# Optimization experiments

Hardware: AMD Instinct MI355X
Metric: run time of the kernel (lower is better)

## Reference

```python
import jax, jax.numpy as jnp
import numpy as np
from jax import lax

VOCAB = 32000
D = 256      # d_model
N = 16       # n_neurons
NL = 6       # n_layers
DS = 16      # d_state
DC = 4       # d_conv
DI = 512     # d_inner = expand * d_model
DTR = 16     # dt_rank = ceil(D/16)
NH = 4       # attention heads
HD = D // NH
B, L = 1, 128


def setup_inputs() -> dict:
    key = jax.random.key(0)
    ks = list(jax.random.split(key, 32))
    it = iter(ks)

    def rn(shape, scale):
        return jax.random.normal(next(it), shape, jnp.float32) * scale

    p = {}
    p["x"] = jax.random.randint(next(it), (B, L), 0, VOCAB, dtype=jnp.int32)
    p["embedding"] = rn((VOCAB, D), 0.02)
    p["norm1_w"] = jnp.ones((NL, D)); p["norm1_b"] = jnp.zeros((NL, D))
    p["norm2_w"] = jnp.ones((NL, D)); p["norm2_b"] = jnp.zeros((NL, D))
    # Mamba params (stacked over layers)
    p["in_proj_w"] = rn((NL, 2 * DI, D), D ** -0.5)
    p["conv_w"] = rn((NL, DI, DC), DC ** -0.5)
    p["conv_b"] = jnp.zeros((NL, DI))
    p["x_proj_w"] = rn((NL, DTR + 2 * DS, DI), DI ** -0.5)
    p["dt_proj_w"] = rn((NL, DI, DTR), DTR ** -0.5)
    dt0 = jax.random.uniform(next(it), (NL, DI), jnp.float32, 1e-3, 1e-1)
    p["dt_proj_b"] = jnp.log(jnp.expm1(dt0))  # inverse softplus init
    p["A_log"] = jnp.log(jnp.tile(jnp.arange(1.0, DS + 1.0, dtype=jnp.float32), (NL, DI, 1)))
    p["skip_D"] = jnp.ones((NL, DI))
    p["out_proj_w"] = rn((NL, D, DI), DI ** -0.5)
    # cross-neuron MHA params
    p["attn_in_w"] = rn((NL, 3 * D, D), D ** -0.5)
    p["attn_in_b"] = jnp.zeros((NL, 3 * D))
    p["attn_out_w"] = rn((NL, D, D), D ** -0.5)
    p["attn_out_b"] = jnp.zeros((NL, D))
    p["norm_f_w"] = jnp.ones((D,)); p["norm_f_b"] = jnp.zeros((D,))
    p["head_b"] = jnp.zeros((VOCAB,))
    return p


def _ln(x, w, b):
    m = x.mean(-1, keepdims=True)
    v = ((x - m) ** 2).mean(-1, keepdims=True)
    return (x - m) * lax.rsqrt(v + 1e-5) * w + b


def _mamba(x, ipw, cw, cb, xpw, dpw, dpb, alog, dskip, opw):
    # x: (BN, L, D)
    BN, Ls, _ = x.shape
    xz = x @ ipw.T                       # (BN, L, 2*DI)
    u, z = xz[..., :DI], xz[..., DI:]
    # depthwise causal conv1d, kernel DC, left-pad DC-1
    uc = lax.conv_general_dilated(
        u.swapaxes(1, 2), cw[:, None, :], (1,), [(DC - 1, 0)],
        dimension_numbers=("NCH", "OIH", "NCH"), feature_group_count=DI)
    u = jax.nn.silu(uc + cb[None, :, None]).swapaxes(1, 2)  # (BN, L, DI)
    xdbl = u @ xpw.T                     # (BN, L, DTR+2*DS)
    dt = jax.nn.softplus(xdbl[..., :DTR] @ dpw.T + dpb)     # (BN, L, DI)
    Bm = xdbl[..., DTR:DTR + DS]
    Cm = xdbl[..., DTR + DS:]
    A = -jnp.exp(alog)                   # (DI, DS)

    def step(h, ins):
        dt_t, b_t, c_t, u_t = ins        # (BN,DI) (BN,DS) (BN,DS) (BN,DI)
        h = jnp.exp(dt_t[..., None] * A) * h + (dt_t * u_t)[..., None] * b_t[:, None, :]
        return h, jnp.einsum("bds,bs->bd", h, c_t)

    h0 = jnp.zeros((BN, DI, DS), x.dtype)
    _, ys = lax.scan(step, h0, (dt.swapaxes(0, 1), Bm.swapaxes(0, 1),
                                Cm.swapaxes(0, 1), u.swapaxes(0, 1)))
    y = ys.swapaxes(0, 1) + u * dskip
    return (y * jax.nn.silu(z)) @ opw.T


def _mha(x, iw, ib, ow, ob):
    # x: (B*L, N, D); self-attention across neurons
    Bq, S, _ = x.shape
    qkv = x @ iw.T + ib
    q, k, v = jnp.split(qkv, 3, axis=-1)
    q = q.reshape(Bq, S, NH, HD); k = k.reshape(Bq, S, NH, HD); v = v.reshape(Bq, S, NH, HD)
    att = jax.nn.softmax(jnp.einsum("bqhd,bkhd->bhqk", q, k) / np.float32(np.sqrt(HD)), axis=-1)
    o = jnp.einsum("bhqk,bkhd->bqhd", att, v).reshape(Bq, S, D)
    return o @ ow.T + ob


def reference(x, embedding, norm1_w, norm1_b, norm2_w, norm2_b, in_proj_w, conv_w,
              conv_b, x_proj_w, dt_proj_w, dt_proj_b, A_log, skip_D, out_proj_w,
              attn_in_w, attn_in_b, attn_out_w, attn_out_b, norm_f_w, norm_f_b, head_b):
    Bb, Ll = x.shape
    h = embedding[x]                                             # (B, L, D)
    h = jnp.broadcast_to(h[:, None], (Bb, N, Ll, D)).reshape(Bb * N, Ll, D)
    for i in range(NL):
        h = h + _mamba(_ln(h, norm1_w[i], norm1_b[i]), in_proj_w[i], conv_w[i],
                       conv_b[i], x_proj_w[i], dt_proj_w[i], dt_proj_b[i],
                       A_log[i], skip_D[i], out_proj_w[i])
        xc = _ln(h, norm2_w[i], norm2_b[i]).reshape(Bb, N, Ll, D)
        xc = xc.transpose(0, 2, 1, 3).reshape(Bb * Ll, N, D)
        co = _mha(xc, attn_in_w[i], attn_in_b[i], attn_out_w[i], attn_out_b[i])
        h = h + co.reshape(Bb, Ll, N, D).transpose(0, 2, 1, 3).reshape(Bb * N, Ll, D)
    h = h.reshape(Bb, N, Ll, D).mean(axis=1)                     # avg over neurons
    return _ln(h, norm_f_w, norm_f_b) @ embedding.T + head_b     # tied head
```

## Files before the change

kernel.cpp:

```cpp
#include <hip/hip_runtime.h>

constexpr int SEQ    = 128;
constexpr int NVOCAB = 32000;

constexpr size_t O_HA = 0;
constexpr size_t O_HB = O_HA + (size_t)SEQ*256;
constexpr size_t O_U  = O_HB + (size_t)SEQ*256;
constexpr size_t O_DT = O_U  + (size_t)SEQ*512;
constexpr size_t O_ZS = O_DT + (size_t)SEQ*512;
constexpr size_t O_BC = O_ZS + (size_t)SEQ*512;
constexpr size_t O_YG = O_BC + (size_t)SEQ*32;
constexpr size_t O_AH = O_YG + (size_t)SEQ*512;

__device__ __forceinline__ float wsum(float p) {
    #pragma unroll
    for (int m = 1; m < 64; m <<= 1) p += __shfl_xor(p, m);
    return p;
}
__device__ __forceinline__ float dot4(float4 a, float4 b) {
    return a.x*b.x + a.y*b.y + a.z*b.z + a.w*b.w;
}

template<int MR, int KK, int S>
__device__ __forceinline__ void gemm3(
    const float* __restrict__ Wg, const float* __restrict__ A, int AS,
    float* __restrict__ dest, int DS,
    const float* __restrict__ addsrc, int ASS, const float* __restrict__ bias)
{
    constexpr int NST = KK / (4 * S);
    const int tid = threadIdx.x;
    const int tq  = tid & (S - 1);
    const int c0  = (tid / S) * 2;
    const float* Wp0 = Wg + (size_t)c0*KK + tq*4;
    const float* Wp1 = Wp0 + KK;

    float acc0[MR], acc1[MR];
    #pragma unroll
    for (int r = 0; r < MR; ++r) { acc0[r] = 0.f; acc1[r] = 0.f; }

    float4 wa0 = *(const float4*)(Wp0);
    float4 wa1 = *(const float4*)(Wp1);
    float4 wb0 = *(const float4*)(Wp0 + 4*S);
    float4 wb1 = *(const float4*)(Wp1 + 4*S);

    #pragma unroll 1
    for (int st = 0; st < NST; st += 2) {
        float4 na0, na1, nb0, nb1;
        const bool pa = (st + 2 < NST);
        const bool pb = (st + 3 < NST);
        if (pa) { na0 = *(const float4*)(Wp0 + (st+2)*4*S);
                  na1 = *(const float4*)(Wp1 + (st+2)*4*S); }
        if (pb) { nb0 = *(const float4*)(Wp0 + (st+3)*4*S);
                  nb1 = *(const float4*)(Wp1 + (st+3)*4*S); }
        const int k0 = st*4*S + tq*4;
        #pragma unroll
        for (int r = 0; r < MR; ++r) {
            float4 a = *(const float4*)&A[r*AS + k0];
            acc0[r] += dot4(a, wa0);
            acc1[r] += dot4(a, wa1);
        }
        const int k1 = k0 + 4*S;
        #pragma unroll
        for (int r = 0; r < MR; ++r) {
            float4 a = *(const float4*)&A[r*AS + k1];
            acc0[r] += dot4(a, wb0);
            acc1[r] += dot4(a, wb1);
        }
        if (pa) { wa0 = na0; wa1 = na1; }
        if (pb) { wb0 = nb0; wb1 = nb1; }
    }
    #pragma unroll
    for (int m = 1; m < S; m <<= 1) {
        #pragma unroll
        for (int r = 0; r < MR; ++r) {
            acc0[r] += __shfl_xor(acc0[r], m);
            acc1[r] += __shfl_xor(acc1[r], m);
        }
    }
    if (tq == 0) {
        #pragma unroll
        for (int r = 0; r < MR; ++r) {
            float ox = acc0[r], oy = acc1[r];
            if (bias) { ox += bias[c0]; oy += bias[c0+1]; }
            if (addsrc) {
                float2 s = *(const float2*)&addsrc[r*ASS + c0];
                ox += s.x; oy += s.y;
            }
            float2 o; o.x = ox; o.y = oy;
            *(float2*)&dest[r*DS + c0] = o;
        }
    }
}

__device__ __forceinline__ void ln_row(const float* __restrict__ src, float* __restrict__ dst,
                                       const float* __restrict__ w, const float* __restrict__ b)
{
    int lane = threadIdx.x & 63;
    float4 x = *(const float4*)&src[lane*4];
    float sm = wsum(x.x + x.y + x.z + x.w);
    float mean = sm * (1.0f/256.0f);
    float d0 = x.x-mean, d1 = x.y-mean, d2 = x.z-mean, d3 = x.w-mean;
    float var = wsum(d0*d0 + d1*d1 + d2*d2 + d3*d3) * (1.0f/256.0f);
    float rstd = rsqrtf(var + 1e-5f);
    float4 ww = *(const float4*)&w[lane*4];
    float4 bb = *(const float4*)&b[lane*4];
    float4 o;
    o.x = d0*rstd*ww.x + bb.x;
    o.y = d1*rstd*ww.y + bb.y;
    o.z = d2*rstd*ww.z + bb.z;
    o.w = d3*rstd*ww.w + bb.w;
    *(float4*)&dst[lane*4] = o;
}

__global__ __launch_bounds__(1024, 4) void rowk_kernel(
    const int* __restrict__ x, const float* __restrict__ emb,
    const float* __restrict__ n1w_l, const float* __restrict__ n1b_l,
    const float* __restrict__ n2w_l, const float* __restrict__ n2b_l,
    const float* __restrict__ ipw_l, const float* __restrict__ cw_l, const float* __restrict__ cb_l,
    const float* __restrict__ xpw_l, const float* __restrict__ dpw_l, const float* __restrict__ dpb_l,
    const float* __restrict__ opw_l, const float* __restrict__ aivw_l, const float* __restrict__ aivb_l,
    const float* __restrict__ aow_l, const float* __restrict__ aob_l,
    const float* __restrict__ nfw, const float* __restrict__ nfb,
    const float* __restrict__ hin, float* __restrict__ hout,
    const float* __restrict__ ygv, float* __restrict__ uv, float* __restrict__ dtv,
    float* __restrict__ zsv, float* __restrict__ bcv, float* __restrict__ AH,
    int li)
{
    __shared__ float SM[6336];
    float* hP  = SM;
    float* h1  = SM + 1056;
    float* sLN = SM + 2112;
    float* sAX = SM + 3168;
    float* zR  = SM + 5248;
    float* suR = SM + 5760;
    float* sxR = SM + 6272;

    const int r = blockIdx.x;
    const int tid = threadIdx.x;
    const int lane = tid & 63, wv = tid >> 6;
    int rr[4];
    #pragma unroll
    for (int j = 0; j < 4; ++j) { int v = r - 3 + j; rr[j] = v < 0 ? 0 : v; }

    {
        int hr = tid >> 8, hc = tid & 255;
        if (li <= 1) hP[hr*264 + hc] = emb[(size_t)x[rr[hr]]*256 + hc];
        else         hP[hr*264 + hc] = hin[rr[hr]*256 + hc];
    }
    if (li >= 1) {
        int yr = tid >> 9, yc = tid & 511;
        sAX[yr*520 + yc]     = ygv[rr[yr]*512 + yc];
        sAX[(2+yr)*520 + yc] = ygv[rr[2+yr]*512 + yc];
    }
    __syncthreads();

    float* hC = hP;
    if (li >= 1) {
        gemm3<4,512,8>(opw_l, sAX, 520, h1, 264, hP, 264, nullptr);
        __syncthreads();
        if (wv < 4) ln_row(h1 + wv*264, sLN + wv*264, n2w_l, n2b_l);
        __syncthreads();
        gemm3<4,256,8>(aivw_l, sLN, 264, sAX, 520, nullptr, 0, aivb_l);
        __syncthreads();
        gemm3<4,256,8>(aow_l, sAX, 520, h1, 264, h1, 264, aob_l);
        __syncthreads();
        hC = h1;
        if (tid < 256) hout[r*256 + tid] = h1[3*264 + tid];
        if (li == 6) {
            if (tid < 256) {
                float v = h1[3*264 + tid];
                float s = wsum(v);
                float q = wsum(v*v);
                if (lane == 0) { sxR[wv] = s; sxR[8 + wv] = q; }
            }
            __syncthreads();
            if (tid < 256) {
                float v = h1[3*264 + tid];
                float mean = (sxR[0]+sxR[1]+sxR[2]+sxR[3]) * (1.0f/256.0f);
                float var  = (sxR[8]+sxR[9]+sxR[10]+sxR[11]) * (1.0f/256.0f) - mean*mean;
                float rstd = rsqrtf(var + 1e-5f);
                AH[r*256 + tid] = (v - mean)*rstd*nfw[tid] + nfb[tid];
            }
            return;
        }
    }

    if (wv < 4) ln_row(hC + wv*264, sLN + wv*264, n1w_l, n1b_l);
    __syncthreads();
    gemm3<4,256,4>(ipw_l,                   sLN,         264, sAX, 520, nullptr, 0, nullptr);
    gemm3<1,256,4>(ipw_l + (size_t)512*256, sLN + 3*264, 264, zR,  512, nullptr, 0, nullptr);
    __syncthreads();

    if (tid < 512) {
        int d = tid;
        float4 c4 = *(const float4*)&cw_l[d*4];
        float acc = cb_l[d];
        if (r >= 3) acc += sAX[d]        * c4.x;
        if (r >= 2) acc += sAX[520 + d]  * c4.y;
        if (r >= 1) acc += sAX[1040 + d] * c4.z;
        acc += sAX[1560 + d] * c4.w;
        float sg = acc / (1.0f + __expf(-acc));
        suR[d] = sg;
        uv[r*512 + d] = sg;
        float z = zR[d];
        zsv[r*512 + d] = z / (1.0f + __expf(-z));
    }
    __syncthreads();

    {
        float4 a0 = *(const float4*)&suR[lane*4];
        float4 a1 = *(const float4*)&suR[256 + lane*4];
        float p[3];
        #pragma unroll
        for (int j = 0; j < 3; ++j) {
            int c = wv*3 + j;
            float4 q0 = *(const float4*)&xpw_l[(size_t)c*512 + lane*4];
            float4 q1 = *(const float4*)&xpw_l[(size_t)c*512 + 256 + lane*4];
            p[j] = dot4(a0, q0) + dot4(a1, q1);
        }
        #pragma unroll
        for (int m = 1; m < 64; m <<= 1) {
            #pragma unroll
            for (int j = 0; j < 3; ++j) p[j] += __shfl_xor(p[j], m);
        }
        if (lane == 0) {
            #pragma unroll
            for (int j = 0; j < 3; ++j) sxR[wv*3 + j] = p[j];
        }
    }
    __syncthreads();
    if (tid >= 16 && tid < 48) bcv[r*32 + tid - 16] = sxR[tid];

    if (tid < 512) {
        int d = tid;
        float4 sx0 = *(const float4*)&sxR[0];
        float4 sx1 = *(const float4*)&sxR[4];
        float4 sx2 = *(const float4*)&sxR[8];
        float4 sx3 = *(const float4*)&sxR[12];
        const float4* dp = (const float4*)&dpw_l[(size_t)d*16];
        float acc = dpb_l[d] + dot4(dp[0], sx0) + dot4(dp[1], sx1)
                             + dot4(dp[2], sx2) + dot4(dp[3], sx3);
        dtv[r*512 + d] = fmaxf(acc, 0.0f) + log1pf(__expf(-fabsf(acc)));
    }
}

__global__ __launch_bounds__(128) void scan_kernel(
    const float* __restrict__ dt, const float* __restrict__ u, const float* __restrict__ zs,
    const float* __restrict__ bcv,
    const float* __restrict__ alog_l, const float* __restrict__ dsk_l,
    float* __restrict__ yg)
{
    __shared__ float sdt[8*132];
    __shared__ float su2[8*132];
    __shared__ float sz2[8*132];
    __shared__ float sB [16*132];
    __shared__ float sC [16*132];
    const int tid = threadIdx.x;
    const int s  = tid & 15;
    const int dl = tid >> 4;
    const int d0 = blockIdx.x * 8;
    const int d  = d0 + dl;

    {
        const int t = tid;
        float4 q0, q1;
        q0 = *(const float4*)&dt[t*512 + d0];
        q1 = *(const float4*)&dt[t*512 + d0 + 4];
        sdt[0*132+t]=q0.x; sdt[1*132+t]=q0.y; sdt[2*132+t]=q0.z; sdt[3*132+t]=q0.w;
        sdt[4*132+t]=q1.x; sdt[5*132+t]=q1.y; sdt[6*132+t]=q1.z; sdt[7*132+t]=q1.w;
        q0 = *(const float4*)&u[t*512 + d0];
        q1 = *(const float4*)&u[t*512 + d0 + 4];
        su2[0*132+t]=q0.x; su2[1*132+t]=q0.y; su2[2*132+t]=q0.z; su2[3*132+t]=q0.w;
        su2[4*132+t]=q1.x; su2[5*132+t]=q1.y; su2[6*132+t]=q1.z; su2[7*132+t]=q1.w;
        q0 = *(const float4*)&zs[t*512 + d0];
        q1 = *(const float4*)&zs[t*512 + d0 + 4];
        sz2[0*132+t]=q0.x; sz2[1*132+t]=q0.y; sz2[2*132+t]=q0.z; sz2[3*132+t]=q0.w;
        sz2[4*132+t]=q1.x; sz2[5*132+t]=q1.y; sz2[6*132+t]=q1.z; sz2[7*132+t]=q1.w;
        float4 b0 = *(const float4*)&bcv[t*32 + 0];
        float4 b1 = *(const float4*)&bcv[t*32 + 4];
        float4 b2 = *(const float4*)&bcv[t*32 + 8];
        float4 b3 = *(const float4*)&bcv[t*32 + 12];
        sB[ 0*132+t]=b0.x; sB[ 1*132+t]=b0.y; sB[ 2*132+t]=b0.z; sB[ 3*132+t]=b0.w;
        sB[ 4*132+t]=b1.x; sB[ 5*132+t]=b1.y; sB[ 6*132+t]=b1.z; sB[ 7*132+t]=b1.w;
        sB[ 8*132+t]=b2.x; sB[ 9*132+t]=b2.y; sB[10*132+t]=b2.z; sB[11*132+t]=b2.w;
        sB[12*132+t]=b3.x; sB[13*132+t]=b3.y; sB[14*132+t]=b3.z; sB[15*132+t]=b3.w;
        float4 c0 = *(const float4*)&bcv[t*32 + 16];
        float4 c1 = *(const float4*)&bcv[t*32 + 20];
        float4 c2 = *(const float4*)&bcv[t*32 + 24];
        float4 c3 = *(const float4*)&bcv[t*32 + 28];
        sC[ 0*132+t]=c0.x; sC[ 1*132+t]=c0.y; sC[ 2*132+t]=c0.z; sC[ 3*132+t]=c0.w;
        sC[ 4*132+t]=c1.x; sC[ 5*132+t]=c1.y; sC[ 6*132+t]=c1.z; sC[ 7*132+t]=c1.w;
        sC[ 8*132+t]=c2.x; sC[ 9*132+t]=c2.y; sC[10*132+t]=c2.z; sC[11*132+t]=c2.w;
        sC[12*132+t]=c3.x; sC[13*132+t]=c3.y; sC[14*132+t]=c3.z; sC[15*132+t]=c3.w;
    }
    __syncthreads();

    const float a_ds = -__expf(alog_l[d*16 + s]);
    const float dskv = dsk_l[d];
    float hst = 0.0f;
    #pragma unroll 8
    for (int t = 0; t < SEQ; ++t) {
        float dtvv = sdt[dl*132 + t];
        float uvv  = su2[dl*132 + t];
        hst = __expf(dtvv * a_ds) * hst + dtvv * uvv * sB[s*132 + t];
        float p = hst * sC[s*132 + t];
        p += __shfl_xor(p, 1);
        p += __shfl_xor(p, 2);
        p += __shfl_xor(p, 4);
        p += __shfl_xor(p, 8);
        if (s == 0) yg[t*512 + d] = (p + uvv * dskv) * sz2[dl*132 + t];
    }
}

__global__ __launch_bounds__(256) void head_kernel(
    const float* __restrict__ AH, const float* __restrict__ emb,
    const float* __restrict__ hb, float* __restrict__ out)
{
    __shared__ float sA[32*132];
    __shared__ float sW[32*68];
    const int tid = threadIdx.x;
    const int c0  = blockIdx.x * 64;
    const int ar = tid >> 1;
    const int ak = (tid & 1) * 16;
    const int wc = tid & 63;
    const int wk = (tid >> 6) * 8;
    const int rg = tid >> 4;
    const int cg = tid & 15;

    const float* Ap = AH  + (size_t)ar*256 + ak;
    const float* Wp = emb + (size_t)(c0 + wc)*256 + wk;

    float4 ra0 = *(const float4*)(Ap + 0);
    float4 ra1 = *(const float4*)(Ap + 4);
    float4 ra2 = *(const float4*)(Ap + 8);
    float4 ra3 = *(const float4*)(Ap + 12);
    float4 rw0 = *(const float4*)(Wp + 0);
    float4 rw1 = *(const float4*)(Wp + 4);

    float acc[8][4] = {};

    for (int kc = 0; kc < 256; kc += 32) {
        if (kc) __syncthreads();
        sA[(ak+ 0)*132+ar]=ra0.x; sA[(ak+ 1)*132+ar]=ra0.y; sA[(ak+ 2)*132+ar]=ra0.z; sA[(ak+ 3)*132+ar]=ra0.w;
        sA[(ak+ 4)*132+ar]=ra1.x; sA[(ak+ 5)*132+ar]=ra1.y; sA[(ak+ 6)*132+ar]=ra1.z; sA[(ak+ 7)*132+ar]=ra1.w;
        sA[(ak+ 8)*132+ar]=ra2.x; sA[(ak+ 9)*132+ar]=ra2.y; sA[(ak+10)*132+ar]=ra2.z; sA[(ak+11)*132+ar]=ra2.w;
        sA[(ak+12)*132+ar]=ra3.x; sA[(ak+13)*132+ar]=ra3.y; sA[(ak+14)*132+ar]=ra3.z; sA[(ak+15)*132+ar]=ra3.w;
        sW[(wk+0)*68+wc]=rw0.x; sW[(wk+1)*68+wc]=rw0.y; sW[(wk+2)*68+wc]=rw0.z; sW[(wk+3)*68+wc]=rw0.w;
        sW[(wk+4)*68+wc]=rw1.x; sW[(wk+5)*68+wc]=rw1.y; sW[(wk+6)*68+wc]=rw1.z; sW[(wk+7)*68+wc]=rw1.w;
        __syncthreads();
        if (kc + 32 < 256) {
            ra0 = *(const float4*)(Ap + kc + 32);
            ra1 = *(const float4*)(Ap + kc + 36);
            ra2 = *(const float4*)(Ap + kc + 40);
            ra3 = *(const float4*)(Ap + kc + 44);
            rw0 = *(const float4*)(Wp + kc + 32);
            rw1 = *(const float4*)(Wp + kc + 36);
        }
        #pragma unroll
        for (int k = 0; k < 32; ++k) {
            float4 a0 = *(const float4*)&sA[k*132 + rg*8];
            float4 a1 = *(const float4*)&sA[k*132 + rg*8 + 4];
            float4 b  = *(const float4*)&sW[k*68  + cg*4];
            float av[8] = {a0.x,a0.y,a0.z,a0.w, a1.x,a1.y,a1.z,a1.w};
            #pragma unroll
            for (int i = 0; i < 8; ++i) {
                acc[i][0] += av[i]*b.x;
                acc[i][1] += av[i]*b.y;
                acc[i][2] += av[i]*b.z;
                acc[i][3] += av[i]*b.w;
            }
        }
    }

    const int c = c0 + cg*4;
    float4 h4 = *(const float4*)&hb[c];
    #pragma unroll
    for (int i = 0; i < 8; ++i) {
        int r = rg*8 + i;
        float4 o;
        o.x = acc[i][0] + h4.x;
        o.y = acc[i][1] + h4.y;
        o.z = acc[i][2] + h4.z;
        o.w = acc[i][3] + h4.w;
        *(float4*)&out[(size_t)r*NVOCAB + c] = o;
    }
}

extern "C" void kernel_launch(void* const* d_in, const int* in_sizes, int n_in,
                              void* d_out, int out_size, void* d_ws, size_t ws_size,
                              hipStream_t stream)
{
    const int*   xin = (const int*)d_in[0];
    const float* emb = (const float*)d_in[1];
    const float* n1w = (const float*)d_in[2];
    const float* n1b = (const float*)d_in[3];
    const float* n2w = (const float*)d_in[4];
    const float* n2b = (const float*)d_in[5];
    const float* ipw = (const float*)d_in[6];
    const float* cw  = (const float*)d_in[7];
    const float* cb  = (const float*)d_in[8];
    const float* xpw = (const float*)d_in[9];
    const float* dpw = (const float*)d_in[10];
    const float* dpb = (const float*)d_in[11];
    const float* alog= (const float*)d_in[12];
    const float* dsk = (const float*)d_in[13];
    const float* opw = (const float*)d_in[14];
    const float* aiw = (const float*)d_in[15];
    const float* aib = (const float*)d_in[16];
    const float* aow = (const float*)d_in[17];
    const float* aob = (const float*)d_in[18];
    const float* nfw = (const float*)d_in[19];
    const float* nfb = (const float*)d_in[20];
    const float* hb  = (const float*)d_in[21];
    float* ws  = (float*)d_ws;
    float* out = (float*)d_out;

    for (int i = 0; i <= 6; ++i) {
        int ka = i <= 5 ? i : 5;
        int kc = i >= 1 ? i - 1 : 0;
        const float* hin  = (i % 2 == 0) ? ws + O_HA : ws + O_HB;
        float*       hout = (i % 2 == 0) ? ws + O_HB : ws + O_HA;
        rowk_kernel<<<128, 1024, 0, stream>>>(
            xin, emb,
            n1w + ka*256, n1b + ka*256,
            n2w + kc*256, n2b + kc*256,
            ipw + (size_t)ka*1024*256, cw + (size_t)ka*512*4, cb + ka*512,
            xpw + (size_t)ka*48*512, dpw + (size_t)ka*512*16, dpb + ka*512,
            opw + (size_t)kc*256*512,
            aiw + (size_t)kc*768*256 + (size_t)512*256, aib + kc*768 + 512,
            aow + (size_t)kc*256*256, aob + kc*256,
            nfw, nfb,
            hin, hout,
            ws + O_YG, ws + O_U, ws + O_DT, ws + O_ZS, ws + O_BC, ws + O_AH,
            i);
        if (i <= 5)
            scan_kernel<<<64, 128, 0, stream>>>(
                ws + O_DT, ws + O_U, ws + O_ZS, ws + O_BC,
                alog + (size_t)i*512*16, dsk + i*512, ws + O_YG);
    }
    head_kernel<<<NVOCAB/64, 256, 0, stream>>>(ws + O_AH, emb, hb, out);
}
```

Measured before the change: 558.9 us.

## Fold attention V and output projections into one matrix; split scan over more blocks

Result: slower. 596.6 us (+6.7%).

```diff
diff --git a/kernel.cpp b/kernel.cpp
--- a/kernel.cpp
+++ b/kernel.cpp
@@ -11,6 +11,8 @@
 constexpr size_t O_BC = O_ZS + (size_t)SEQ*512;
 constexpr size_t O_YG = O_BC + (size_t)SEQ*32;
 constexpr size_t O_AH = O_YG + (size_t)SEQ*512;
+constexpr size_t O_WC = O_AH + (size_t)SEQ*256;
+constexpr size_t O_BB = O_WC + (size_t)6*256*256;
 
 __device__ __forceinline__ float wsum(float p) {
     #pragma unroll
@@ -19,6 +21,51 @@
 }
 __device__ __forceinline__ float dot4(float4 a, float4 b) {
     return a.x*b.x + a.y*b.y + a.z*b.z + a.w*b.w;
+}
+
+__global__ __launch_bounds__(256) void combo_kernel(
+    const float* __restrict__ aiw, const float* __restrict__ aib,
+    const float* __restrict__ aow, const float* __restrict__ aob,
+    float* __restrict__ wc, float* __restrict__ bc)
+{
+    const int l   = blockIdx.x >> 4;
+    const int c0  = (blockIdx.x & 15) * 16;
+    const int tid = threadIdx.x;
+    const int c   = c0 + (tid >> 4);
+    const int k0  = (tid & 15) * 16;
+    const float* av = aiw + (size_t)l*768*256 + (size_t)512*256;
+    const float* ab = aib + l*768 + 512;
+    const float* ow = aow + (size_t)l*256*256;
+    const float* ob = aob + l*256;
+
+    float4 acc[4] = {};
+    for (int j0 = 0; j0 < 256; j0 += 4) {
+        float4 a4 = *(const float4*)&ow[(size_t)c*256 + j0];
+        #pragma unroll
+        for (int jj = 0; jj < 4; ++jj) {
+            float aj = (&a4.x)[jj];
+            const float* wrow = av + (size_t)(j0+jj)*256 + k0;
+            #pragma unroll
+            for (int q = 0; q < 4; ++q) {
+                float4 w4 = *(const float4*)(wrow + q*4);
+                acc[q].x += aj*w4.x; acc[q].y += aj*w4.y;
+                acc[q].z += aj*w4.z; acc[q].w += aj*w4.w;
+            }
+        }
+    }
+    float* wout = wc + (size_t)l*256*256 + (size_t)c*256 + k0;
+    #pragma unroll
+    for (int q = 0; q < 4; ++q) *(float4*)(wout + q*4) = acc[q];
+
+    if ((tid & 15) == 0) {
+        float b = ob[c];
+        for (int j0 = 0; j0 < 256; j0 += 4) {
+            float4 a4 = *(const float4*)&ow[(size_t)c*256 + j0];
+            float4 b4 = *(const float4*)&ab[j0];
+            b += a4.x*b4.x + a4.y*b4.y + a4.z*b4.z + a4.w*b4.w;
+        }
+        bc[l*256 + c] = b;
+    }
 }
 
 template<int MR, int KK, int S>
@@ -118,8 +165,7 @@
     const float* __restrict__ n2w_l, const float* __restrict__ n2b_l,
     const float* __restrict__ ipw_l, const float* __restrict__ cw_l, const float* __restrict__ cb_l,
     const float* __restrict__ xpw_l, const float* __restrict__ dpw_l, const float* __restrict__ dpb_l,
-    const float* __restrict__ opw_l, const float* __restrict__ aivw_l, const float* __restrict__ aivb_l,
-    const float* __restrict__ aow_l, const float* __restrict__ aob_l,
+    const float* __restrict__ opw_l, const float* __restrict__ wc_l, const float* __restrict__ bc_l,
     const float* __restrict__ nfw, const float* __restrict__ nfb,
     const float* __restrict__ hin, float* __restrict__ hout,
     const float* __restrict__ ygv, float* __restrict__ uv, float* __restrict__ dtv,
@@ -160,9 +206,7 @@
         __syncthreads();
         if (wv < 4) ln_row(h1 + wv*264, sLN + wv*264, n2w_l, n2b_l);
         __syncthreads();
-        gemm3<4,256,8>(aivw_l, sLN, 264, sAX, 520, nullptr, 0, aivb_l);
-        __syncthreads();
-        gemm3<4,256,8>(aow_l, sAX, 520, h1, 264, h1, 264, aob_l);
+        gemm3<4,256,8>(wc_l, sLN, 264, h1, 264, h1, 264, bc_l);
         __syncthreads();
         hC = h1;
         if (tid < 256) hout[r*256 + tid] = h1[3*264 + tid];
@@ -244,38 +288,33 @@
     }
 }
 
-__global__ __launch_bounds__(128) void scan_kernel(
+__global__ __launch_bounds__(64) void scan_kernel(
     const float* __restrict__ dt, const float* __restrict__ u, const float* __restrict__ zs,
     const float* __restrict__ bcv,
     const float* __restrict__ alog_l, const float* __restrict__ dsk_l,
     float* __restrict__ yg)
 {
-    __shared__ float sdt[8*132];
-    __shared__ float su2[8*132];
-    __shared__ float sz2[8*132];
+    __shared__ float sdt[4*132];
+    __shared__ float su2[4*132];
+    __shared__ float sz2[4*132];
     __shared__ float sB [16*132];
     __shared__ float sC [16*132];
     const int tid = threadIdx.x;
     const int s  = tid & 15;
     const int dl = tid >> 4;
-    const int d0 = blockIdx.x * 8;
+    const int d0 = blockIdx.x * 4;
     const int d  = d0 + dl;
 
-    {
-        const int t = tid;
-        float4 q0, q1;
-        q0 = *(const float4*)&dt[t*512 + d0];
-        q1 = *(const float4*)&dt[t*512 + d0 + 4];
-        sdt[0*132+t]=q0.x; sdt[1*132+t]=q0.y; sdt[2*132+t]=q0.z; sdt[3*132+t]=q0.w;
-        sdt[4*132+t]=q1.x; sdt[5*132+t]=q1.y; sdt[6*132+t]=q1.z; sdt[7*132+t]=q1.w;
-        q0 = *(const float4*)&u[t*512 + d0];
-        q1 = *(const float4*)&u[t*512 + d0 + 4];
-        su2[0*132+t]=q0.x; su2[1*132+t]=q0.y; su2[2*132+t]=q0.z; su2[3*132+t]=q0.w;
-        su2[4*132+t]=q1.x; su2[5*132+t]=q1.y; su2[6*132+t]=q1.z; su2[7*132+t]=q1.w;
-        q0 = *(const float4*)&zs[t*512 + d0];
-        q1 = *(const float4*)&zs[t*512 + d0 + 4];
-        sz2[0*132+t]=q0.x; sz2[1*132+t]=q0.y; sz2[2*132+t]=q0.z; sz2[3*132+t]=q0.w;
-        sz2[4*132+t]=q1.x; sz2[5*132+t]=q1.y; sz2[6*132+t]=q1.z; sz2[7*132+t]=q1.w;
+    #pragma unroll
+    for (int tt = 0; tt < 2; ++tt) {
+        const int t = tid + tt*64;
+        float4 q;
+        q = *(const float4*)&dt[t*512 + d0];
+        sdt[0*132+t]=q.x; sdt[1*132+t]=q.y; sdt[2*132+t]=q.z; sdt[3*132+t]=q.w;
+        q = *(const float4*)&u[t*512 + d0];
+        su2[0*132+t]=q.x; su2[1*132+t]=q.y; su2[2*132+t]=q.z; su2[3*132+t]=q.w;
+        q = *(const float4*)&zs[t*512 + d0];
+        sz2[0*132+t]=q.x; sz2[1*132+t]=q.y; sz2[2*132+t]=q.z; sz2[3*132+t]=q.w;
         float4 b0 = *(const float4*)&bcv[t*32 + 0];
         float4 b1 = *(const float4*)&bcv[t*32 + 4];
         float4 b2 = *(const float4*)&bcv[t*32 + 8];
@@ -415,6 +454,8 @@
     float* ws  = (float*)d_ws;
     float* out = (float*)d_out;
 
+    combo_kernel<<<96, 256, 0, stream>>>(aiw, aib, aow, aob, ws + O_WC, ws + O_BB);
+
     for (int i = 0; i <= 6; ++i) {
         int ka = i <= 5 ? i : 5;
         int kc = i >= 1 ? i - 1 : 0;
@@ -427,14 +468,13 @@
             ipw + (size_t)ka*1024*256, cw + (size_t)ka*512*4, cb + ka*512,
             xpw + (size_t)ka*48*512, dpw + (size_t)ka*512*16, dpb + ka*512,
             opw + (size_t)kc*256*512,
-            aiw + (size_t)kc*768*256 + (size_t)512*256, aib + kc*768 + 512,
-            aow + (size_t)kc*256*256, aob + kc*256,
+            ws + O_WC + (size_t)kc*256*256, ws + O_BB + kc*256,
             nfw, nfb,
             hin, hout,
             ws + O_YG, ws + O_U, ws + O_DT, ws + O_ZS, ws + O_BC, ws + O_AH,
             i);
         if (i <= 5)
-            scan_kernel<<<64, 128, 0, stream>>>(
+            scan_kernel<<<128, 64, 0, stream>>>(
                 ws + O_DT, ws + O_U, ws + O_ZS, ws + O_BC,
                 alog + (size_t)i*512*16, dsk + i*512, ws + O_YG);
     }
```
